# Kernel tuning notes

Measured on AMD Instinct MI355X. Metric: run time of the kernel, lower is better.

Reference implementation:

```python
import jax, jax.numpy as jnp
import numpy as np

D_KEY = 128

def setup_inputs() -> dict:
    key = jax.random.key(0)
    k1, k2, k3, k4 = jax.random.split(key, 4)
    B, S, D = 4, 4096, 1024
    inp = jax.random.normal(k1, (B, S, D), dtype=jnp.float32)
    # torch Linear weight layout: [out_features, in_features]
    Wq = jax.random.normal(k2, (D_KEY, D), dtype=jnp.float32) / np.sqrt(D)
    Wk = jax.random.normal(k3, (D_KEY, D), dtype=jnp.float32) / np.sqrt(D)
    Wv = jax.random.normal(k4, (D_KEY, D), dtype=jnp.float32) / np.sqrt(D)
    # causal mask: 0 => masked out (matches masked_fill(mask == 0, -inf))
    mask = jnp.tril(jnp.ones((S, S), dtype=jnp.int32))
    return {"input": inp, "Wq": Wq, "Wk": Wk, "Wv": Wv, "mask": mask}

def reference(input, Wq, Wk, Wv, mask):
    # projections (no bias, eval mode -> no weight noise)
    q = jnp.einsum('bsd,kd->bsk', input, Wq)  # [B,S,d_key]
    k = jnp.einsum('bsd,kd->bsk', input, Wk)
    v = jnp.einsum('bsd,kd->bsk', input, Wv)
    attn = jnp.einsum('bqk,bsk->bqs', q, k)   # [B,S,S]
    attn = jnp.where(mask == 0, -jnp.inf, attn)
    scale = np.float32(np.sqrt(D_KEY))
    p = jax.nn.softmax(attn / scale, axis=-1)
    return jnp.einsum('bqs,bsk->bqk', p, v)   # [B,S,d_key]
```

## Files before the change

### kernel.cpp

```cpp
#include <hip/hip_runtime.h>
#include <hip/hip_bf16.h>

typedef __bf16 bf16_t;
typedef bf16_t bf16x8 __attribute__((ext_vector_type(8)));
typedef bf16_t bf16x4 __attribute__((ext_vector_type(4)));
typedef float  f32x4  __attribute__((ext_vector_type(4)));

#define LOG2E    1.4426950408889634f
#define QK_SCALE 0.08838834764831845f

static constexpr int BB = 4, SS = 4096, DD = 1024, DK = 128;

static constexpr size_t WB_OFF = 0;
static constexpr size_t Q_OFF  = 1u << 20;
static constexpr size_t K_OFF  = Q_OFF + (size_t)BB * SS * DK * 2;
static constexpr size_t VT_OFF = K_OFF + (size_t)BB * SS * DK * 2;

__global__ __launch_bounds__(256) void wconv_kernel(const float* __restrict__ Wq,
                                                    const float* __restrict__ Wk,
                                                    const float* __restrict__ Wv,
                                                    bf16_t* __restrict__ wb) {
    int i4 = blockIdx.x * 256 + threadIdx.x;
    int e  = i4 * 4;
    const float* src = (e < 131072) ? Wq : (e < 262144 ? Wk : Wv);
    int off = e & 131071;
    f32x4 v = *(const f32x4*)(src + off);
    bf16x4 o = { (bf16_t)v[0], (bf16_t)v[1], (bf16_t)v[2], (bf16_t)v[3] };
    *(bf16x4*)(wb + e) = o;
}

__global__ __launch_bounds__(256) void proj_kernel(const float* __restrict__ inp,
                                                   const bf16_t* __restrict__ wb,
                                                   bf16_t* __restrict__ qo,
                                                   bf16_t* __restrict__ ko,
                                                   bf16_t* __restrict__ vto) {
    __shared__ bf16_t At[128][72];
    __shared__ bf16_t Wt[128][72];

    const int tid = threadIdx.x;
    const int w = tid >> 6, lane = tid & 63;
    const int lr = lane & 15, lh = lane >> 4;
    const int m0 = blockIdx.x * 128;
    const int y  = blockIdx.y;

    f32x4 acc[2][8] = {};

    for (int k0 = 0; k0 < DD; k0 += 64) {
        #pragma unroll
        for (int i = 0; i < 8; ++i) {
            int fi  = tid + i * 256;
            int row = fi >> 4, c4 = (fi & 15) * 4;
            f32x4 v = *(const f32x4*)(inp + (size_t)(m0 + row) * DD + k0 + c4);
            bf16x4 bv = { (bf16_t)v[0], (bf16_t)v[1], (bf16_t)v[2], (bf16_t)v[3] };
            *(bf16x4*)&At[row][c4] = bv;
        }
        #pragma unroll
        for (int i = 0; i < 4; ++i) {
            int uu = tid + i * 256;
            int wr = uu >> 3, uc = (uu & 7) * 8;
            *(bf16x8*)&Wt[wr][uc] = *(const bf16x8*)(wb + (size_t)(y * 128 + wr) * DD + k0 + uc);
        }
        __syncthreads();
        #pragma unroll
        for (int kk = 0; kk < 64; kk += 32) {
            bf16x8 a0 = *(const bf16x8*)&At[w * 32      + lr][kk + lh * 8];
            bf16x8 a1 = *(const bf16x8*)&At[w * 32 + 16 + lr][kk + lh * 8];
            #pragma unroll
            for (int ct = 0; ct < 8; ++ct) {
                bf16x8 wf = *(const bf16x8*)&Wt[ct * 16 + lr][kk + lh * 8];
                acc[0][ct] = __builtin_amdgcn_mfma_f32_16x16x32_bf16(a0, wf, acc[0][ct], 0, 0, 0);
                acc[1][ct] = __builtin_amdgcn_mfma_f32_16x16x32_bf16(a1, wf, acc[1][ct], 0, 0, 0);
            }
        }
        __syncthreads();
    }

    if (y < 2) {
        bf16_t* out = (y == 0) ? qo : ko;
        #pragma unroll
        for (int rt = 0; rt < 2; ++rt)
            #pragma unroll
            for (int ct = 0; ct < 8; ++ct)
                #pragma unroll
                for (int r = 0; r < 4; ++r) {
                    int m = m0 + w * 32 + rt * 16 + lh * 4 + r;
                    out[(size_t)m * DK + ct * 16 + lr] = (bf16_t)acc[rt][ct][r];
                }
    } else {
        int b = m0 >> 12;
        int sbase = (m0 & 4095) + w * 32;
        #pragma unroll
        for (int rt = 0; rt < 2; ++rt)
            #pragma unroll
            for (int ct = 0; ct < 8; ++ct) {
                bf16x4 pk = { (bf16_t)acc[rt][ct][0], (bf16_t)acc[rt][ct][1],
                              (bf16_t)acc[rt][ct][2], (bf16_t)acc[rt][ct][3] };
                int s = sbase + rt * 16 + lh * 4;
                *(bf16x4*)(vto + (size_t)b * DK * SS + (size_t)(ct * 16 + lr) * SS + s) = pk;
            }
    }
}

__global__ __launch_bounds__(256) void attn_kernel(const bf16_t* __restrict__ q,
                                                   const bf16_t* __restrict__ k,
                                                   const bf16_t* __restrict__ vt,
                                                   float* __restrict__ out) {
    __shared__ bf16_t Pl[4][32][72];
    __shared__ float  ml[4][32][2];
    __shared__ float  Osh[32][128];

    const int tid = threadIdx.x, w = tid >> 6, lane = tid & 63;
    const int lr = lane & 15, lh = lane >> 4;
    const int b  = blockIdx.x >> 7;
    const int t  = blockIdx.x & 127;
    const int q0 = t * 32;
    const int NT = (q0 + 31) / 64 + 1;

    const bf16_t* qb = q  + (size_t)b * SS * DK;
    const bf16_t* kb = k  + (size_t)b * SS * DK;
    const bf16_t* vb = vt + (size_t)b * DK * SS;

    bf16x8 qf[2][4];
    #pragma unroll
    for (int rt = 0; rt < 2; ++rt)
        #pragma unroll
        for (int kc = 0; kc < 4; ++kc)
            qf[rt][kc] = *(const bf16x8*)(qb + (size_t)(q0 + rt * 16 + lr) * DK + kc * 32 + lh * 8);

    f32x4 oacc[2][8] = {};
    float mv[2][4], lv[2][4];
    #pragma unroll
    for (int rt = 0; rt < 2; ++rt)
        #pragma unroll
        for (int r = 0; r < 4; ++r) { mv[rt][r] = -INFINITY; lv[rt][r] = 0.f; }

    for (int kt = w; kt < NT; kt += 4) {
        const int kvb = kt * 64;
        f32x4 sf[2][4] = {};
        #pragma unroll
        for (int ct = 0; ct < 4; ++ct) {
            bf16x8 kf[4];
            #pragma unroll
            for (int kc = 0; kc < 4; ++kc)
                kf[kc] = *(const bf16x8*)(kb + (size_t)(kvb + ct * 16 + lr) * DK + kc * 32 + lh * 8);
            #pragma unroll
            for (int rt = 0; rt < 2; ++rt)
                #pragma unroll
                for (int kc = 0; kc < 4; ++kc)
                    sf[rt][ct] = __builtin_amdgcn_mfma_f32_16x16x32_bf16(qf[rt][kc], kf[kc], sf[rt][ct], 0, 0, 0);
        }
        const bool need_mask = (kvb + 63 > q0);
        #pragma unroll
        for (int rt = 0; rt < 2; ++rt) {
            float alpha[4];
            #pragma unroll
            for (int r = 0; r < 4; ++r) {
                float vals[4];
                float mx = -INFINITY;
                #pragma unroll
                for (int ct = 0; ct < 4; ++ct) {
                    float v = sf[rt][ct][r] * QK_SCALE;
                    if (need_mask) {
                        int kv_g = kvb + ct * 16 + lr;
                        int q_g  = q0 + rt * 16 + lh * 4 + r;
                        if (kv_g > q_g) v = -INFINITY;
                    }
                    vals[ct] = v;
                    mx = fmaxf(mx, v);
                }
                mx = fmaxf(mx, __shfl_xor(mx, 1));
                mx = fmaxf(mx, __shfl_xor(mx, 2));
                mx = fmaxf(mx, __shfl_xor(mx, 4));
                mx = fmaxf(mx, __shfl_xor(mx, 8));
                float mnew = fmaxf(mv[rt][r], mx);
                float al   = exp2f((mv[rt][r] - mnew) * LOG2E);
                mv[rt][r]  = mnew;
                float rs = 0.f;
                #pragma unroll
                for (int ct = 0; ct < 4; ++ct) {
                    float p = exp2f((vals[ct] - mnew) * LOG2E);
                    rs += p;
                    Pl[w][rt * 16 + lh * 4 + r][ct * 16 + lr] = (bf16_t)p;
                }
                rs += __shfl_xor(rs, 1);
                rs += __shfl_xor(rs, 2);
                rs += __shfl_xor(rs, 4);
                rs += __shfl_xor(rs, 8);
                lv[rt][r] = lv[rt][r] * al + rs;
                alpha[r] = al;
            }
            #pragma unroll
            for (int dt = 0; dt < 8; ++dt)
                #pragma unroll
                for (int r = 0; r < 4; ++r)
                    oacc[rt][dt][r] *= alpha[r];
        }
        bf16x8 pa[2][2];
        #pragma unroll
        for (int rt = 0; rt < 2; ++rt)
            #pragma unroll
            for (int kc = 0; kc < 2; ++kc)
                pa[rt][kc] = *(const bf16x8*)&Pl[w][rt * 16 + lr][kc * 32 + lh * 8];
        #pragma unroll
        for (int dt = 0; dt < 8; ++dt) {
            const bf16_t* vrow = vb + (size_t)(dt * 16 + lr) * SS + kvb + lh * 8;
            bf16x8 vf0 = *(const bf16x8*)(vrow);
            bf16x8 vf1 = *(const bf16x8*)(vrow + 32);
            #pragma unroll
            for (int rt = 0; rt < 2; ++rt) {
                oacc[rt][dt] = __builtin_amdgcn_mfma_f32_16x16x32_bf16(pa[rt][0], vf0, oacc[rt][dt], 0, 0, 0);
                oacc[rt][dt] = __builtin_amdgcn_mfma_f32_16x16x32_bf16(pa[rt][1], vf1, oacc[rt][dt], 0, 0, 0);
            }
        }
    }

    if (lr == 0) {
        #pragma unroll
        for (int rt = 0; rt < 2; ++rt)
            #pragma unroll
            for (int r = 0; r < 4; ++r) {
                int row = rt * 16 + lh * 4 + r;
                ml[w][row][0] = mv[rt][r];
                ml[w][row][1] = lv[rt][r];
            }
    }
    #pragma unroll
    for (int i = 0; i < 4; ++i) {
        int u = tid + i * 256;
        *(f32x4*)&Osh[u >> 5][(u & 31) * 4] = f32x4{0.f, 0.f, 0.f, 0.f};
    }
    __syncthreads();
    #pragma unroll
    for (int rt = 0; rt < 2; ++rt)
        #pragma unroll
        for (int r = 0; r < 4; ++r) {
            int row = rt * 16 + lh * 4 + r;
            float M = fmaxf(fmaxf(ml[0][row][0], ml[1][row][0]),
                            fmaxf(ml[2][row][0], ml[3][row][0]));
            float sc = exp2f((mv[rt][r] - M) * LOG2E);
            #pragma unroll
            for (int dt = 0; dt < 8; ++dt)
                atomicAdd(&Osh[row][dt * 16 + lr], oacc[rt][dt][r] * sc);
        }
    __syncthreads();
    float* ob = out + ((size_t)b * SS + q0) * DK;
    #pragma unroll
    for (int i = 0; i < 4; ++i) {
        int u = tid + i * 256;
        int row = u >> 5, c = (u & 31) * 4;
        float M = fmaxf(fmaxf(ml[0][row][0], ml[1][row][0]),
                        fmaxf(ml[2][row][0], ml[3][row][0]));
        float L = 0.f;
        #pragma unroll
        for (int ww = 0; ww < 4; ++ww)
            L = fmaf(ml[ww][row][1], exp2f((ml[ww][row][0] - M) * LOG2E), L);
        f32x4 o = *(const f32x4*)&Osh[row][c];
        f32x4 res = { o[0] / L, o[1] / L, o[2] / L, o[3] / L };
        *(f32x4*)(ob + (size_t)row * DK + c) = res;
    }
}

extern "C" void kernel_launch(void* const* d_in, const int* in_sizes, int n_in,
                              void* d_out, int out_size, void* d_ws, size_t ws_size,
                              hipStream_t stream) {
    const float* inp = (const float*)d_in[0];
    const float* Wq  = (const float*)d_in[1];
    const float* Wk  = (const float*)d_in[2];
    const float* Wv  = (const float*)d_in[3];

    char* ws = (char*)d_ws;
    bf16_t* wb  = (bf16_t*)(ws + WB_OFF);
    bf16_t* qw  = (bf16_t*)(ws + Q_OFF);
    bf16_t* kw  = (bf16_t*)(ws + K_OFF);
    bf16_t* vtw = (bf16_t*)(ws + VT_OFF);
    float*  o   = (float*)d_out;

    wconv_kernel<<<384, 256, 0, stream>>>(Wq, Wk, Wv, wb);
    proj_kernel<<<dim3(128, 3), 256, 0, stream>>>(inp, wb, qw, kw, vtw);
    attn_kernel<<<512, 256, 0, stream>>>(qw, kw, vtw, o);
}
```

Measured before the change: 334.4 us.

## Fold softmax scale into Wq, shrink projection tiles, widen attention to 8 waves

The QK scale and log2e factor are folded into the bf16 Wq conversion, which removes per-element multiplies in the attention softmax. The projection kernel now uses 64-row tiles with a 2x2 wave split, doubling the grid to 768 blocks to fill the CUs better. The attention kernel runs 8 waves per block that split the KV tiles, processes the heaviest causal query tiles first, and tightens the tile count. Pre-scaling Q before rounding to bf16 shifts rounding slightly, and the 8-way merge adds LDS and atomic work.

```diff
diff --git a/kernel.cpp b/kernel.cpp
--- a/kernel.cpp
+++ b/kernel.cpp
@@ -23,9 +23,11 @@
     int i4 = blockIdx.x * 256 + threadIdx.x;
     int e  = i4 * 4;
     const float* src = (e < 131072) ? Wq : (e < 262144 ? Wk : Wv);
+    float scale = (e < 131072) ? (QK_SCALE * LOG2E) : 1.0f;
     int off = e & 131071;
     f32x4 v = *(const f32x4*)(src + off);
-    bf16x4 o = { (bf16_t)v[0], (bf16_t)v[1], (bf16_t)v[2], (bf16_t)v[3] };
+    bf16x4 o = { (bf16_t)(v[0] * scale), (bf16_t)(v[1] * scale),
+                 (bf16_t)(v[2] * scale), (bf16_t)(v[3] * scale) };
     *(bf16x4*)(wb + e) = o;
 }
 
@@ -34,40 +36,41 @@
                                                    bf16_t* __restrict__ qo,
                                                    bf16_t* __restrict__ ko,
                                                    bf16_t* __restrict__ vto) {
-    __shared__ bf16_t At[128][72];
+    __shared__ bf16_t At[64][72];
     __shared__ bf16_t Wt[128][72];
 
     const int tid = threadIdx.x;
     const int w = tid >> 6, lane = tid & 63;
     const int lr = lane & 15, lh = lane >> 4;
-    const int m0 = blockIdx.x * 128;
+    const int wr = w >> 1, wc = w & 1;
+    const int m0 = blockIdx.x * 64;
     const int y  = blockIdx.y;
 
-    f32x4 acc[2][8] = {};
+    f32x4 acc[2][4] = {};
 
     for (int k0 = 0; k0 < DD; k0 += 64) {
         #pragma unroll
-        for (int i = 0; i < 8; ++i) {
-            int fi  = tid + i * 256;
-            int row = fi >> 4, c4 = (fi & 15) * 4;
+        for (int i = 0; i < 4; ++i) {
+            int u   = tid + i * 256;
+            int row = u >> 4, c4 = (u & 15) * 4;
             f32x4 v = *(const f32x4*)(inp + (size_t)(m0 + row) * DD + k0 + c4);
             bf16x4 bv = { (bf16_t)v[0], (bf16_t)v[1], (bf16_t)v[2], (bf16_t)v[3] };
             *(bf16x4*)&At[row][c4] = bv;
         }
         #pragma unroll
         for (int i = 0; i < 4; ++i) {
-            int uu = tid + i * 256;
-            int wr = uu >> 3, uc = (uu & 7) * 8;
-            *(bf16x8*)&Wt[wr][uc] = *(const bf16x8*)(wb + (size_t)(y * 128 + wr) * DD + k0 + uc);
+            int u  = tid + i * 256;
+            int wrow = u >> 3, uc = (u & 7) * 8;
+            *(bf16x8*)&Wt[wrow][uc] = *(const bf16x8*)(wb + (size_t)(y * 128 + wrow) * DD + k0 + uc);
         }
         __syncthreads();
         #pragma unroll
         for (int kk = 0; kk < 64; kk += 32) {
-            bf16x8 a0 = *(const bf16x8*)&At[w * 32      + lr][kk + lh * 8];
-            bf16x8 a1 = *(const bf16x8*)&At[w * 32 + 16 + lr][kk + lh * 8];
-            #pragma unroll
-            for (int ct = 0; ct < 8; ++ct) {
-                bf16x8 wf = *(const bf16x8*)&Wt[ct * 16 + lr][kk + lh * 8];
+            bf16x8 a0 = *(const bf16x8*)&At[wr * 32      + lr][kk + lh * 8];
+            bf16x8 a1 = *(const bf16x8*)&At[wr * 32 + 16 + lr][kk + lh * 8];
+            #pragma unroll
+            for (int ct = 0; ct < 4; ++ct) {
+                bf16x8 wf = *(const bf16x8*)&Wt[wc * 64 + ct * 16 + lr][kk + lh * 8];
                 acc[0][ct] = __builtin_amdgcn_mfma_f32_16x16x32_bf16(a0, wf, acc[0][ct], 0, 0, 0);
                 acc[1][ct] = __builtin_amdgcn_mfma_f32_16x16x32_bf16(a1, wf, acc[1][ct], 0, 0, 0);
             }
@@ -80,41 +83,42 @@
         #pragma unroll
         for (int rt = 0; rt < 2; ++rt)
             #pragma unroll
-            for (int ct = 0; ct < 8; ++ct)
+            for (int ct = 0; ct < 4; ++ct)
                 #pragma unroll
                 for (int r = 0; r < 4; ++r) {
-                    int m = m0 + w * 32 + rt * 16 + lh * 4 + r;
-                    out[(size_t)m * DK + ct * 16 + lr] = (bf16_t)acc[rt][ct][r];
+                    int m = m0 + wr * 32 + rt * 16 + lh * 4 + r;
+                    out[(size_t)m * DK + wc * 64 + ct * 16 + lr] = (bf16_t)acc[rt][ct][r];
                 }
     } else {
         int b = m0 >> 12;
-        int sbase = (m0 & 4095) + w * 32;
-        #pragma unroll
-        for (int rt = 0; rt < 2; ++rt)
-            #pragma unroll
-            for (int ct = 0; ct < 8; ++ct) {
+        int sbase = (m0 & 4095) + wr * 32;
+        #pragma unroll
+        for (int rt = 0; rt < 2; ++rt)
+            #pragma unroll
+            for (int ct = 0; ct < 4; ++ct) {
                 bf16x4 pk = { (bf16_t)acc[rt][ct][0], (bf16_t)acc[rt][ct][1],
                               (bf16_t)acc[rt][ct][2], (bf16_t)acc[rt][ct][3] };
                 int s = sbase + rt * 16 + lh * 4;
-                *(bf16x4*)(vto + (size_t)b * DK * SS + (size_t)(ct * 16 + lr) * SS + s) = pk;
-            }
-    }
-}
-
-__global__ __launch_bounds__(256) void attn_kernel(const bf16_t* __restrict__ q,
-                                                   const bf16_t* __restrict__ k,
-                                                   const bf16_t* __restrict__ vt,
-                                                   float* __restrict__ out) {
-    __shared__ bf16_t Pl[4][32][72];
-    __shared__ float  ml[4][32][2];
+                int d = wc * 64 + ct * 16 + lr;
+                *(bf16x4*)(vto + (size_t)b * DK * SS + (size_t)d * SS + s) = pk;
+            }
+    }
+}
+
+__global__ __launch_bounds__(512, 4) void attn_kernel(const bf16_t* __restrict__ q,
+                                                      const bf16_t* __restrict__ k,
+                                                      const bf16_t* __restrict__ vt,
+                                                      float* __restrict__ out) {
+    __shared__ bf16_t Pl[8][32][72];
+    __shared__ float  ml[8][32][2];
     __shared__ float  Osh[32][128];
 
     const int tid = threadIdx.x, w = tid >> 6, lane = tid & 63;
     const int lr = lane & 15, lh = lane >> 4;
     const int b  = blockIdx.x >> 7;
-    const int t  = blockIdx.x & 127;
+    const int t  = 127 - (blockIdx.x & 127);
     const int q0 = t * 32;
-    const int NT = (q0 + 31) / 64 + 1;
+    const int NT = q0 / 64 + 1;
 
     const bf16_t* qb = q  + (size_t)b * SS * DK;
     const bf16_t* kb = k  + (size_t)b * SS * DK;
@@ -134,7 +138,7 @@
         #pragma unroll
         for (int r = 0; r < 4; ++r) { mv[rt][r] = -INFINITY; lv[rt][r] = 0.f; }
 
-    for (int kt = w; kt < NT; kt += 4) {
+    for (int kt = w; kt < NT; kt += 8) {
         const int kvb = kt * 64;
         f32x4 sf[2][4] = {};
         #pragma unroll
@@ -159,7 +163,7 @@
                 float mx = -INFINITY;
                 #pragma unroll
                 for (int ct = 0; ct < 4; ++ct) {
-                    float v = sf[rt][ct][r] * QK_SCALE;
+                    float v = sf[rt][ct][r];
                     if (need_mask) {
                         int kv_g = kvb + ct * 16 + lr;
                         int q_g  = q0 + rt * 16 + lh * 4 + r;
@@ -173,12 +177,12 @@
                 mx = fmaxf(mx, __shfl_xor(mx, 4));
                 mx = fmaxf(mx, __shfl_xor(mx, 8));
                 float mnew = fmaxf(mv[rt][r], mx);
-                float al   = exp2f((mv[rt][r] - mnew) * LOG2E);
+                float al   = exp2f(mv[rt][r] - mnew);
                 mv[rt][r]  = mnew;
                 float rs = 0.f;
                 #pragma unroll
                 for (int ct = 0; ct < 4; ++ct) {
-                    float p = exp2f((vals[ct] - mnew) * LOG2E);
+                    float p = exp2f(vals[ct] - mnew);
                     rs += p;
                     Pl[w][rt * 16 + lh * 4 + r][ct * 16 + lr] = (bf16_t)p;
                 }
@@ -225,8 +229,8 @@
             }
     }
     #pragma unroll
-    for (int i = 0; i < 4; ++i) {
-        int u = tid + i * 256;
+    for (int i = 0; i < 2; ++i) {
+        int u = tid + i * 512;
         *(f32x4*)&Osh[u >> 5][(u & 31) * 4] = f32x4{0.f, 0.f, 0.f, 0.f};
     }
     __syncthreads();
@@ -235,9 +239,10 @@
         #pragma unroll
         for (int r = 0; r < 4; ++r) {
             int row = rt * 16 + lh * 4 + r;
-            float M = fmaxf(fmaxf(ml[0][row][0], ml[1][row][0]),
-                            fmaxf(ml[2][row][0], ml[3][row][0]));
-            float sc = exp2f((mv[rt][r] - M) * LOG2E);
+            float M = ml[0][row][0];
+            #pragma unroll
+            for (int ww = 1; ww < 8; ++ww) M = fmaxf(M, ml[ww][row][0]);
+            float sc = exp2f(mv[rt][r] - M);
             #pragma unroll
             for (int dt = 0; dt < 8; ++dt)
                 atomicAdd(&Osh[row][dt * 16 + lr], oacc[rt][dt][r] * sc);
@@ -245,15 +250,16 @@
     __syncthreads();
     float* ob = out + ((size_t)b * SS + q0) * DK;
     #pragma unroll
-    for (int i = 0; i < 4; ++i) {
-        int u = tid + i * 256;
+    for (int i = 0; i < 2; ++i) {
+        int u = tid + i * 512;
         int row = u >> 5, c = (u & 31) * 4;
-        float M = fmaxf(fmaxf(ml[0][row][0], ml[1][row][0]),
-                        fmaxf(ml[2][row][0], ml[3][row][0]));
+        float M = ml[0][row][0];
+        #pragma unroll
+        for (int ww = 1; ww < 8; ++ww) M = fmaxf(M, ml[ww][row][0]);
         float L = 0.f;
         #pragma unroll
-        for (int ww = 0; ww < 4; ++ww)
-            L = fmaf(ml[ww][row][1], exp2f((ml[ww][row][0] - M) * LOG2E), L);
+        for (int ww = 0; ww < 8; ++ww)
+            L = fmaf(ml[ww][row][1], exp2f(ml[ww][row][0] - M), L);
         f32x4 o = *(const f32x4*)&Osh[row][c];
         f32x4 res = { o[0] / L, o[1] / L, o[2] / L, o[3] / L };
         *(f32x4*)(ob + (size_t)row * DK + c) = res;
@@ -276,6 +282,6 @@
     float*  o   = (float*)d_out;
 
     wconv_kernel<<<384, 256, 0, stream>>>(Wq, Wk, Wv, wb);
-    proj_kernel<<<dim3(128, 3), 256, 0, stream>>>(inp, wb, qw, kw, vtw);
-    attn_kernel<<<512, 256, 0, stream>>>(qw, kw, vtw, o);
-}
+    proj_kernel<<<dim3(256, 3), 256, 0, stream>>>(inp, wb, qw, kw, vtw);
+    attn_kernel<<<512, 512, 0, stream>>>(qw, kw, vtw, o);
+}
```

Result: slower. 479.7 us (+43.4%).
